# Performance work log

Measured on AMD Instinct MI355X. Metric: run time of the kernel, lower is better.

Reference implementation:

```python
import jax, jax.numpy as jnp
import numpy as np

NUM_HEADS = 8
T = 8  # hardcoded temporal dim in the original forward
MD = 3  # max_displacement -> 7x7 window
EPS = 1e-12  # F.normalize eps


def l2_normalize(x, axis):
    n = jnp.sqrt(jnp.sum(x * x, axis=axis, keepdims=True))
    return x / jnp.maximum(n, EPS)


def correlation_7x7(q, k):
    # q, k: [B, C, H, W]; FlowNet-style correlation, kernel_size=1, max_disp=3.
    # out[b, u, v, h, w] = sum_c q[b,c,h,w] * k[b,c,h+u-3,w+v-3] (zero padded)
    B, C, H, W = q.shape
    kp = jnp.pad(k, ((0, 0), (0, 0), (MD, MD), (MD, MD)))
    outs = []
    for dy in range(2 * MD + 1):
        for dx in range(2 * MD + 1):
            ks = kp[:, :, dy:dy + H, dx:dx + W]
            outs.append(jnp.sum(q * ks, axis=1))  # [B, H, W]
    corr = jnp.stack(outs, axis=1)  # [B, 49, H, W]
    return corr.reshape(B, 2 * MD + 1, 2 * MD + 1, H, W)


def setup_inputs() -> dict:
    key = jax.random.key(0)
    ks = jax.random.split(key, 6)
    B, N, C = 8, 8192, 256
    hd = C // NUM_HEADS
    std = 0.02
    return {
        "x": jax.random.normal(ks[0], (B, N, C), dtype=jnp.float32),
        "w_qk": jax.random.normal(ks[1], (2 * C, C), dtype=jnp.float32) * std,
        "w_corr": jax.random.normal(ks[2], (hd, 49), dtype=jnp.float32) * std,
        "b_corr": jnp.zeros((hd,), dtype=jnp.float32),
        "w_proj": jax.random.normal(ks[3], (C, C), dtype=jnp.float32) * std,
        "b_proj": jnp.zeros((C,), dtype=jnp.float32),
    }


def reference(x, w_qk, w_corr, b_corr, w_proj, b_proj):
    B, N, C = x.shape
    nh = NUM_HEADS
    hd = C // nh
    H = int(np.sqrt(N // T))
    W = H

    # qk projection (no bias): [B, N, 2C] -> q, k each [B, nh, N, hd]
    qk = jnp.einsum('bnc,dc->bnd', x, w_qk)
    qk = qk.reshape(B, N, 2, nh, hd).transpose(2, 0, 3, 1, 4)
    q, k = qk[0], qk[1]

    # 'b n (t h w) d -> (b n) t d h w'
    q = q.reshape(B * nh, T, H, W, hd).transpose(0, 1, 4, 2, 3)
    k = k.reshape(B * nh, T, H, W, hd).transpose(0, 1, 4, 2, 3)

    # temporal postfix: k[t+1], last frame repeated
    k_post = jnp.concatenate([k[:, 1:], k[:, -1:]], axis=1)

    qp = q.reshape(B * nh * T, hd, H, W)
    kp = k_post.reshape(B * nh * T, hd, H, W)
    qp = l2_normalize(qp, axis=1)
    kp = l2_normalize(kp, axis=1)

    corr = correlation_7x7(qp, kp)  # [(B nh T), 7, 7, H, W]
    # 'b u v h w -> b (h w) (u v)'
    corr = corr.transpose(0, 3, 4, 1, 2).reshape(B * nh * T, H * W, 49)

    v = jnp.einsum('bpk,dk->bpd', corr, w_corr) + b_corr  # [(B nh T), HW, hd]

    # '(b n t) (h w) d -> b n (t h w) d' then 'b h n d -> b n (h d)'
    out = v.reshape(B, nh, T * H * W, hd).transpose(0, 2, 1, 3).reshape(B, N, C)
    out = jnp.einsum('bnc,dc->bnd', out, w_proj) + b_proj
    return out
```

## Files before the change

kernel.cpp:

```cpp
#include <hip/hip_runtime.h>

typedef _Float16 half8 __attribute__((ext_vector_type(8)));
typedef _Float16 half2v __attribute__((ext_vector_type(2)));
typedef float float4v __attribute__((ext_vector_type(4)));

__device__ __forceinline__ float dot2acc(unsigned a, unsigned b, float c) {
#if __has_builtin(__builtin_amdgcn_fdot2)
  return __builtin_amdgcn_fdot2(__builtin_bit_cast(half2v, a), __builtin_bit_cast(half2v, b), c, false);
#else
  half2v ha = __builtin_bit_cast(half2v, a);
  half2v hb = __builtin_bit_cast(half2v, b);
  c += (float)ha[0] * (float)hb[0];
  c += (float)ha[1] * (float)hb[1];
  return c;
#endif
}
__device__ __forceinline__ unsigned hscale(unsigned a, float s) {
  half2v ha = __builtin_bit_cast(half2v, a);
  half2v r;
  r[0] = (_Float16)((float)ha[0] * s);
  r[1] = (_Float16)((float)ha[1] * s);
  return __builtin_bit_cast(unsigned, r);
}
__device__ __forceinline__ unsigned pack2(float a, float b) {
  half2v h;
  h[0] = (_Float16)a;
  h[1] = (_Float16)b;
  return __builtin_bit_cast(unsigned, h);
}
__device__ __forceinline__ void gload_lds16(const void* g, void* l) {
  __builtin_amdgcn_global_load_lds((const __attribute__((address_space(1))) unsigned*)g,
                                   (__attribute__((address_space(3))) unsigned*)l, 16, 0, 0);
}

__global__ void cvt_all(const float4* __restrict__ x, const float4* __restrict__ wqk,
                        const float4* __restrict__ wpj,
                        ushort4* __restrict__ x16, ushort4* __restrict__ wqk16,
                        ushort4* __restrict__ wpj16) {
  int b = blockIdx.x;
  const float4* s;
  ushort4* d;
  int i;
  if (b < 16384) { s = x; d = x16; i = b * 256 + threadIdx.x; }
  else if (b < 16512) { s = wqk; d = wqk16; i = (b - 16384) * 256 + threadIdx.x; }
  else { s = wpj; d = wpj16; i = (b - 16512) * 256 + threadIdx.x; }
  float4 v = s[i];
  _Float16 a = (_Float16)v.x, bb = (_Float16)v.y, c = (_Float16)v.z, e = (_Float16)v.w;
  ushort4 o;
  o.x = __builtin_bit_cast(unsigned short, a);
  o.y = __builtin_bit_cast(unsigned short, bb);
  o.z = __builtin_bit_cast(unsigned short, c);
  o.w = __builtin_bit_cast(unsigned short, e);
  d[i] = o;
}

__global__ __launch_bounds__(512, 4)
void gemm_qk(const _Float16* __restrict__ A, const _Float16* __restrict__ Bw,
             _Float16* __restrict__ qo, _Float16* __restrict__ ko) {
  __shared__ _Float16 Ash[2][4096];
  __shared__ _Float16 Bsh[2][8192];
  const int tid = threadIdx.x;
  const int lane = tid & 63, w = tid >> 6;
  const int wm = w >> 2, wn = w & 3;
  const int ml = lane & 15, qd = lane >> 4;
  const int m0 = blockIdx.y * 128, n0 = blockIdx.x * 256;

  float4v acc[4][4];
  float4v z = {0.f, 0.f, 0.f, 0.f};
#pragma unroll
  for (int i = 0; i < 4; ++i)
#pragma unroll
    for (int j = 0; j < 4; ++j) acc[i][j] = z;

  const _Float16* Ap = A + (size_t)m0 * 256;
  const _Float16* Bp = Bw + (size_t)n0 * 256;
  const int rA = tid >> 2, jA = (tid & 3) ^ ((rA >> 1) & 3);
  const int rB1 = (tid + 512) >> 2, jB1 = (tid & 3) ^ ((rB1 >> 1) & 3);

  gload_lds16(Ap + rA * 256 + jA * 8, &Ash[0][(size_t)(w * 64) * 8]);
  gload_lds16(Bp + rA * 256 + jA * 8, &Bsh[0][(size_t)(w * 64) * 8]);
  gload_lds16(Bp + rB1 * 256 + jB1 * 8, &Bsh[0][(size_t)(512 + w * 64) * 8]);
  __syncthreads();

#pragma unroll
  for (int kt = 0; kt < 8; ++kt) {
    const int cur = kt & 1;
    if (kt < 7) {
      const int k0 = (kt + 1) * 32;
      const int nb = cur ^ 1;
      gload_lds16(Ap + rA * 256 + k0 + jA * 8, &Ash[nb][(size_t)(w * 64) * 8]);
      gload_lds16(Bp + rA * 256 + k0 + jA * 8, &Bsh[nb][(size_t)(w * 64) * 8]);
      gload_lds16(Bp + rB1 * 256 + k0 + jB1 * 8, &Bsh[nb][(size_t)(512 + w * 64) * 8]);
    }
    half8 af[4], bf[4];
#pragma unroll
    for (int im = 0; im < 4; ++im) {
      int rr = wm * 64 + im * 16 + ml;
      af[im] = *(const half8*)(&Ash[cur][rr * 32 + (qd ^ ((rr >> 1) & 3)) * 8]);
      int rc = wn * 64 + im * 16 + ml;
      bf[im] = *(const half8*)(&Bsh[cur][rc * 32 + (qd ^ ((rc >> 1) & 3)) * 8]);
    }
#pragma unroll
    for (int im = 0; im < 4; ++im)
#pragma unroll
      for (int in = 0; in < 4; ++in)
        acc[im][in] = __builtin_amdgcn_mfma_f32_16x16x32_f16(bf[in], af[im], acc[im][in], 0, 0, 0);
    __syncthreads();
  }

#pragma unroll
  for (int im = 0; im < 4; ++im) {
    int rowr = m0 + wm * 64 + im * 16 + ml;
    int b = rowr >> 13, n = rowr & 8191;
    int t = n >> 10, yx = n & 1023;
#pragma unroll
    for (int in = 0; in < 4; ++in) {
      int col = n0 + wn * 64 + in * 16 + qd * 4;
      int s = col >> 8, h = (col >> 5) & 7, j = col & 31;
      _Float16* dst = s ? ko : qo;
      int p = b * 64 + h * 8 + t;
      uint2 pk;
      pk.x = pack2(acc[im][in][0], acc[im][in][1]);
      pk.y = pack2(acc[im][in][2], acc[im][in][3]);
      *(uint2*)(dst + ((size_t)p * 1024 + yx) * 32 + j) = pk;
    }
  }
}

__global__ __launch_bounds__(256, 4)
void corr_kernel(const _Float16* __restrict__ q16, const _Float16* __restrict__ k16,
                 const float* __restrict__ wcorr, const float* __restrict__ bcorr,
                 _Float16* __restrict__ outp) {
  __shared__ uint4 smem[2304];
  __shared__ uint4 wcs[256];

  const int tid = threadIdx.x;
  const int bx = blockIdx.x;
  const int p = bx >> 2, tile = bx & 3;
  const int y0 = (tile >> 1) * 16, x0 = (tile & 1) * 16;
  const int b = p >> 6, h = (p >> 3) & 7, t = p & 7;
  const int pk = (t < 7) ? p + 1 : p;
  const int ty = tid >> 4, tx = tid & 15;

  _Float16* wch = (_Float16*)wcs;
  for (int idx = tid; idx < 2048; idx += 256) {
    int d = idx >> 6, kk = idx & 63;
    float v = (kk < 49) ? wcorr[d * 49 + kk] : (kk == 49 ? bcorr[d] : 0.f);
    wch[idx] = (_Float16)v;
  }

  const _Float16* kbase = k16 + (size_t)pk * 32768;
#pragma unroll
  for (int i = 0; i < 8; ++i) {
    int g = tid + i * 256;
    if (g < 1936) {
      int vec = g >> 2, part = g & 3;
      int ky = vec / 22, kx = vec - ky * 22;
      int gy = y0 + ky - 3, gx = x0 + kx - 3;
      uint4 val = make_uint4(0u, 0u, 0u, 0u);
      if (gy >= 0 && gy < 32 && gx >= 0 && gx < 32)
        val = *(const uint4*)(kbase + ((size_t)gy * 32 + gx) * 32 + part * 8);
      int slot = (vec << 2) | (part ^ (vec & 3) ^ ((vec >> 2) & 3));
      smem[slot] = val;
    }
  }
  __syncthreads();

  for (int v = tid; v < 484; v += 256) {
    int base = v << 2;
    int sw = (v & 3) ^ ((v >> 2) & 3);
    uint4 gg[4];
#pragma unroll
    for (int pq = 0; pq < 4; ++pq) gg[pq] = smem[base | (pq ^ sw)];
    float ss = 0.f;
#pragma unroll
    for (int pq = 0; pq < 4; ++pq) {
      const unsigned* u = (const unsigned*)&gg[pq];
#pragma unroll
      for (int e = 0; e < 4; ++e) ss = dot2acc(u[e], u[e], ss);
    }
    float sc = 1.f / fmaxf(sqrtf(ss), 1e-12f);
#pragma unroll
    for (int pq = 0; pq < 4; ++pq) {
      unsigned* u = (unsigned*)&gg[pq];
#pragma unroll
      for (int e = 0; e < 4; ++e) u[e] = hscale(u[e], sc);
      smem[base | (pq ^ sw)] = gg[pq];
    }
  }
  __syncthreads();

  const _Float16* qptr = q16 + (size_t)p * 32768 + ((size_t)(y0 + ty) * 32 + (x0 + tx)) * 32;
  uint4 qv[4];
#pragma unroll
  for (int i = 0; i < 4; ++i) qv[i] = *(const uint4*)(qptr + i * 8);
  unsigned* qu = (unsigned*)qv;
  float qss = 0.f;
#pragma unroll
  for (int e = 0; e < 16; ++e) qss = dot2acc(qu[e], qu[e], qss);
  float qsc = 1.f / fmaxf(sqrtf(qss), 1e-12f);
#pragma unroll
  for (int e = 0; e < 16; ++e) qu[e] = hscale(qu[e], qsc);

  float corr[49];
#pragma unroll
  for (int dy = 0; dy < 7; ++dy) {
#pragma unroll
    for (int dx = 0; dx < 7; ++dx) {
      int vec = (ty + dy) * 22 + (tx + dx);
      int base = vec << 2;
      int sw = (vec & 3) ^ ((vec >> 2) & 3);
      float c = 0.f;
#pragma unroll
      for (int pq = 0; pq < 4; ++pq) {
        uint4 kk = smem[base | (pq ^ sw)];
        const unsigned* ku = (const unsigned*)&kk;
#pragma unroll
        for (int e = 0; e < 4; ++e) c = dot2acc(qu[pq * 4 + e], ku[e], c);
      }
      corr[dy * 7 + dx] = c;
    }
  }
  __syncthreads();

#pragma unroll
  for (int i = 0; i < 8; ++i) {
    uint4 val;
    unsigned* vu = (unsigned*)&val;
#pragma unroll
    for (int e = 0; e < 4; ++e) {
      int idx = i * 8 + e * 2;
      half2v hh;
      hh[0] = (_Float16)(idx < 49 ? corr[idx] : (idx == 49 ? 1.f : 0.f));
      hh[1] = (_Float16)(idx + 1 < 49 ? corr[idx + 1] : (idx + 1 == 49 ? 1.f : 0.f));
      vu[e] = __builtin_bit_cast(unsigned, hh);
    }
    smem[tid * 9 + i] = val;
  }
  __syncthreads();

  _Float16* corrm = (_Float16*)smem;
  const int lane = tid & 63, w = tid >> 6;
  const int ml = lane & 15, qd = lane >> 4;
  float4v vacc[4][2];
  float4v z = {0.f, 0.f, 0.f, 0.f};
#pragma unroll
  for (int im = 0; im < 4; ++im) { vacc[im][0] = z; vacc[im][1] = z; }
#pragma unroll
  for (int ks = 0; ks < 2; ++ks) {
    half8 bfrag[2];
#pragma unroll
    for (int nt = 0; nt < 2; ++nt)
      bfrag[nt] = *(const half8*)(wch + (nt * 16 + ml) * 64 + ks * 32 + qd * 8);
#pragma unroll
    for (int im = 0; im < 4; ++im) {
      half8 afrag = *(const half8*)(corrm + (w * 64 + im * 16 + ml) * 72 + ks * 32 + qd * 8);
#pragma unroll
      for (int nt = 0; nt < 2; ++nt)
        vacc[im][nt] = __builtin_amdgcn_mfma_f32_16x16x32_f16(afrag, bfrag[nt], vacc[im][nt], 0, 0, 0);
    }
  }

#pragma unroll
  for (int im = 0; im < 4; ++im) {
#pragma unroll
    for (int nt = 0; nt < 2; ++nt) {
      int d = nt * 16 + ml;
#pragma unroll
      for (int r = 0; r < 4; ++r) {
        int pos = w * 64 + im * 16 + qd * 4 + r;
        int py = pos >> 4, px = pos & 15;
        int n = t * 1024 + (y0 + py) * 32 + (x0 + px);
        outp[(((size_t)b * 8192 + n) << 8) + h * 32 + d] = (_Float16)vacc[im][nt][r];
      }
    }
  }
}

__global__ __launch_bounds__(512, 4)
void gemm_proj(const _Float16* __restrict__ A, const _Float16* __restrict__ Bw,
               const float* __restrict__ bp, float* __restrict__ out) {
  __shared__ _Float16 Ash[2][4096];
  __shared__ _Float16 Bsh[2][8192];
  const int tid = threadIdx.x;
  const int lane = tid & 63, w = tid >> 6;
  const int wm = w >> 2, wn = w & 3;
  const int ml = lane & 15, qd = lane >> 4;
  const int m0 = blockIdx.x * 128;

  float4v acc[4][4];
  float4v z = {0.f, 0.f, 0.f, 0.f};
#pragma unroll
  for (int i = 0; i < 4; ++i)
#pragma unroll
    for (int j = 0; j < 4; ++j) acc[i][j] = z;

  const _Float16* Ap = A + (size_t)m0 * 256;
  const _Float16* Bp = Bw;
  const int rA = tid >> 2, jA = (tid & 3) ^ ((rA >> 1) & 3);
  const int rB1 = (tid + 512) >> 2, jB1 = (tid & 3) ^ ((rB1 >> 1) & 3);

  gload_lds16(Ap + rA * 256 + jA * 8, &Ash[0][(size_t)(w * 64) * 8]);
  gload_lds16(Bp + rA * 256 + jA * 8, &Bsh[0][(size_t)(w * 64) * 8]);
  gload_lds16(Bp + rB1 * 256 + jB1 * 8, &Bsh[0][(size_t)(512 + w * 64) * 8]);
  __syncthreads();

#pragma unroll
  for (int kt = 0; kt < 8; ++kt) {
    const int cur = kt & 1;
    if (kt < 7) {
      const int k0 = (kt + 1) * 32;
      const int nb = cur ^ 1;
      gload_lds16(Ap + rA * 256 + k0 + jA * 8, &Ash[nb][(size_t)(w * 64) * 8]);
      gload_lds16(Bp + rA * 256 + k0 + jA * 8, &Bsh[nb][(size_t)(w * 64) * 8]);
      gload_lds16(Bp + rB1 * 256 + k0 + jB1 * 8, &Bsh[nb][(size_t)(512 + w * 64) * 8]);
    }
    half8 af[4], bf[4];
#pragma unroll
    for (int im = 0; im < 4; ++im) {
      int rr = wm * 64 + im * 16 + ml;
      af[im] = *(const half8*)(&Ash[cur][rr * 32 + (qd ^ ((rr >> 1) & 3)) * 8]);
      int rc = wn * 64 + im * 16 + ml;
      bf[im] = *(const half8*)(&Bsh[cur][rc * 32 + (qd ^ ((rc >> 1) & 3)) * 8]);
    }
#pragma unroll
    for (int im = 0; im < 4; ++im)
#pragma unroll
      for (int in = 0; in < 4; ++in)
        acc[im][in] = __builtin_amdgcn_mfma_f32_16x16x32_f16(bf[in], af[im], acc[im][in], 0, 0, 0);
    __syncthreads();
  }

#pragma unroll
  for (int im = 0; im < 4; ++im) {
    int rowr = m0 + wm * 64 + im * 16 + ml;
#pragma unroll
    for (int in = 0; in < 4; ++in) {
      int col = wn * 64 + in * 16 + qd * 4;
      float4 bb = *(const float4*)(bp + col);
      float4 o;
      o.x = acc[im][in][0] + bb.x;
      o.y = acc[im][in][1] + bb.y;
      o.z = acc[im][in][2] + bb.z;
      o.w = acc[im][in][3] + bb.w;
      *(float4*)(out + (size_t)rowr * 256 + col) = o;
    }
  }
}

extern "C" void kernel_launch(void* const* d_in, const int* in_sizes, int n_in,
                              void* d_out, int out_size, void* d_ws, size_t ws_size,
                              hipStream_t stream) {
  const float* x      = (const float*)d_in[0];
  const float* w_qk   = (const float*)d_in[1];
  const float* w_corr = (const float*)d_in[2];
  const float* b_corr = (const float*)d_in[3];
  const float* w_proj = (const float*)d_in[4];
  const float* b_proj = (const float*)d_in[5];
  float* out = (float*)d_out;

  char* ws = (char*)d_ws;
  _Float16* x16   = (_Float16*)(ws);
  _Float16* q16   = (_Float16*)(ws + 33554432);
  _Float16* k16   = (_Float16*)(ws + 67108864);
  _Float16* op16  = (_Float16*)(ws + 100663296);
  _Float16* wqk16 = (_Float16*)(ws + 134217728);
  _Float16* wpj16 = (_Float16*)(ws + 134479872);

  cvt_all<<<16576, 256, 0, stream>>>((const float4*)x, (const float4*)w_qk, (const float4*)w_proj,
                                     (ushort4*)x16, (ushort4*)wqk16, (ushort4*)wpj16);
  gemm_qk<<<dim3(2, 512), 512, 0, stream>>>(x16, wqk16, q16, k16);
  corr_kernel<<<2048, 256, 0, stream>>>(q16, k16, w_corr, b_corr, op16);
  gemm_proj<<<512, 512, 0, stream>>>(op16, wpj16, b_proj, out);
}
```

Measured before the change: 225.5 us.

## Fuse x fp32-to-fp16 conversion and L2 normalization into QK GEMM

The fp32 input x is now loaded directly inside the QK GEMM, converted to fp16 in registers and written into the LDS A tile. This removes the separate conversion pass over x and its fp16 round trip through memory. The per-head L2 normalization of q and k also moves into the GEMM epilogue using cross-lane shuffles, so the correlation kernel no longer renormalizes the key halo and query vectors. The cost is that the A-operand loads now go through registers instead of direct global-to-LDS loads, which adds VGPR pressure and LDS store work inside the main loop.

Measured after the change: 215.4 us. 1.05x faster.

```diff
diff --git a/kernel.cpp b/kernel.cpp
--- a/kernel.cpp
+++ b/kernel.cpp
@@ -15,13 +15,6 @@
   return c;
 #endif
 }
-__device__ __forceinline__ unsigned hscale(unsigned a, float s) {
-  half2v ha = __builtin_bit_cast(half2v, a);
-  half2v r;
-  r[0] = (_Float16)((float)ha[0] * s);
-  r[1] = (_Float16)((float)ha[1] * s);
-  return __builtin_bit_cast(unsigned, r);
-}
 __device__ __forceinline__ unsigned pack2(float a, float b) {
   half2v h;
   h[0] = (_Float16)a;
@@ -33,17 +26,14 @@
                                    (__attribute__((address_space(3))) unsigned*)l, 16, 0, 0);
 }
 
-__global__ void cvt_all(const float4* __restrict__ x, const float4* __restrict__ wqk,
-                        const float4* __restrict__ wpj,
-                        ushort4* __restrict__ x16, ushort4* __restrict__ wqk16,
-                        ushort4* __restrict__ wpj16) {
+__global__ void cvt_w(const float4* __restrict__ wqk, const float4* __restrict__ wpj,
+                      ushort4* __restrict__ wqk16, ushort4* __restrict__ wpj16) {
   int b = blockIdx.x;
   const float4* s;
   ushort4* d;
   int i;
-  if (b < 16384) { s = x; d = x16; i = b * 256 + threadIdx.x; }
-  else if (b < 16512) { s = wqk; d = wqk16; i = (b - 16384) * 256 + threadIdx.x; }
-  else { s = wpj; d = wpj16; i = (b - 16512) * 256 + threadIdx.x; }
+  if (b < 128) { s = wqk; d = wqk16; i = b * 256 + threadIdx.x; }
+  else { s = wpj; d = wpj16; i = (b - 128) * 256 + threadIdx.x; }
   float4 v = s[i];
   _Float16 a = (_Float16)v.x, bb = (_Float16)v.y, c = (_Float16)v.z, e = (_Float16)v.w;
   ushort4 o;
@@ -55,7 +45,7 @@
 }
 
 __global__ __launch_bounds__(512, 4)
-void gemm_qk(const _Float16* __restrict__ A, const _Float16* __restrict__ Bw,
+void gemm_qk(const float* __restrict__ X, const _Float16* __restrict__ Bw,
              _Float16* __restrict__ qo, _Float16* __restrict__ ko) {
   __shared__ _Float16 Ash[2][4096];
   __shared__ _Float16 Bsh[2][8192];
@@ -72,25 +62,35 @@
 #pragma unroll
     for (int j = 0; j < 4; ++j) acc[i][j] = z;
 
-  const _Float16* Ap = A + (size_t)m0 * 256;
+  const float* Xp = X + (size_t)m0 * 256;
   const _Float16* Bp = Bw + (size_t)n0 * 256;
-  const int rA = tid >> 2, jA = (tid & 3) ^ ((rA >> 1) & 3);
+  const int ar = tid >> 2, aj = tid & 3;
+  const int ajx = aj ^ ((ar >> 1) & 3);
+  const int rB0 = tid >> 2, jB0 = (tid & 3) ^ ((rB0 >> 1) & 3);
   const int rB1 = (tid + 512) >> 2, jB1 = (tid & 3) ^ ((rB1 >> 1) & 3);
 
-  gload_lds16(Ap + rA * 256 + jA * 8, &Ash[0][(size_t)(w * 64) * 8]);
-  gload_lds16(Bp + rA * 256 + jA * 8, &Bsh[0][(size_t)(w * 64) * 8]);
+  float4 a0 = *(const float4*)(Xp + (size_t)ar * 256 + ajx * 8);
+  float4 a1 = *(const float4*)(Xp + (size_t)ar * 256 + ajx * 8 + 4);
+  gload_lds16(Bp + rB0 * 256 + jB0 * 8, &Bsh[0][(size_t)(w * 64) * 8]);
   gload_lds16(Bp + rB1 * 256 + jB1 * 8, &Bsh[0][(size_t)(512 + w * 64) * 8]);
+  {
+    half8 h;
+    h[0] = (_Float16)a0.x; h[1] = (_Float16)a0.y; h[2] = (_Float16)a0.z; h[3] = (_Float16)a0.w;
+    h[4] = (_Float16)a1.x; h[5] = (_Float16)a1.y; h[6] = (_Float16)a1.z; h[7] = (_Float16)a1.w;
+    *(half8*)(&Ash[0][ar * 32 + aj * 8]) = h;
+  }
   __syncthreads();
 
 #pragma unroll
   for (int kt = 0; kt < 8; ++kt) {
     const int cur = kt & 1;
+    float4 n0f, n1f;
     if (kt < 7) {
       const int k0 = (kt + 1) * 32;
-      const int nb = cur ^ 1;
-      gload_lds16(Ap + rA * 256 + k0 + jA * 8, &Ash[nb][(size_t)(w * 64) * 8]);
-      gload_lds16(Bp + rA * 256 + k0 + jA * 8, &Bsh[nb][(size_t)(w * 64) * 8]);
-      gload_lds16(Bp + rB1 * 256 + k0 + jB1 * 8, &Bsh[nb][(size_t)(512 + w * 64) * 8]);
+      n0f = *(const float4*)(Xp + (size_t)ar * 256 + k0 + ajx * 8);
+      n1f = *(const float4*)(Xp + (size_t)ar * 256 + k0 + ajx * 8 + 4);
+      gload_lds16(Bp + rB0 * 256 + k0 + jB0 * 8, &Bsh[cur ^ 1][(size_t)(w * 64) * 8]);
+      gload_lds16(Bp + rB1 * 256 + k0 + jB1 * 8, &Bsh[cur ^ 1][(size_t)(512 + w * 64) * 8]);
     }
     half8 af[4], bf[4];
 #pragma unroll
@@ -105,6 +105,12 @@
 #pragma unroll
       for (int in = 0; in < 4; ++in)
         acc[im][in] = __builtin_amdgcn_mfma_f32_16x16x32_f16(bf[in], af[im], acc[im][in], 0, 0, 0);
+    if (kt < 7) {
+      half8 h;
+      h[0] = (_Float16)n0f.x; h[1] = (_Float16)n0f.y; h[2] = (_Float16)n0f.z; h[3] = (_Float16)n0f.w;
+      h[4] = (_Float16)n1f.x; h[5] = (_Float16)n1f.y; h[6] = (_Float16)n1f.z; h[7] = (_Float16)n1f.w;
+      *(half8*)(&Ash[cur ^ 1][ar * 32 + aj * 8]) = h;
+    }
     __syncthreads();
   }
 
@@ -114,15 +120,29 @@
     int b = rowr >> 13, n = rowr & 8191;
     int t = n >> 10, yx = n & 1023;
 #pragma unroll
-    for (int in = 0; in < 4; ++in) {
-      int col = n0 + wn * 64 + in * 16 + qd * 4;
-      int s = col >> 8, h = (col >> 5) & 7, j = col & 31;
-      _Float16* dst = s ? ko : qo;
-      int p = b * 64 + h * 8 + t;
-      uint2 pk;
-      pk.x = pack2(acc[im][in][0], acc[im][in][1]);
-      pk.y = pack2(acc[im][in][2], acc[im][in][3]);
-      *(uint2*)(dst + ((size_t)p * 1024 + yx) * 32 + j) = pk;
+    for (int hh = 0; hh < 2; ++hh) {
+      float ss = 0.f;
+#pragma unroll
+      for (int ii = 0; ii < 2; ++ii) {
+        int in = hh * 2 + ii;
+#pragma unroll
+        for (int r = 0; r < 4; ++r) ss += acc[im][in][r] * acc[im][in][r];
+      }
+      ss += __shfl_xor(ss, 16);
+      ss += __shfl_xor(ss, 32);
+      float sc = 1.f / fmaxf(sqrtf(ss), 1e-12f);
+#pragma unroll
+      for (int ii = 0; ii < 2; ++ii) {
+        int in = hh * 2 + ii;
+        int col = n0 + wn * 64 + in * 16 + qd * 4;
+        int s = col >> 8, h = (col >> 5) & 7, j = col & 31;
+        _Float16* dst = s ? ko : qo;
+        int p = b * 64 + h * 8 + t;
+        uint2 pk;
+        pk.x = pack2(acc[im][in][0] * sc, acc[im][in][1] * sc);
+        pk.y = pack2(acc[im][in][2] * sc, acc[im][in][3] * sc);
+        *(uint2*)(dst + ((size_t)p * 1024 + yx) * 32 + j) = pk;
+      }
     }
   }
 }
@@ -164,43 +184,13 @@
       smem[slot] = val;
     }
   }
-  __syncthreads();
-
-  for (int v = tid; v < 484; v += 256) {
-    int base = v << 2;
-    int sw = (v & 3) ^ ((v >> 2) & 3);
-    uint4 gg[4];
-#pragma unroll
-    for (int pq = 0; pq < 4; ++pq) gg[pq] = smem[base | (pq ^ sw)];
-    float ss = 0.f;
-#pragma unroll
-    for (int pq = 0; pq < 4; ++pq) {
-      const unsigned* u = (const unsigned*)&gg[pq];
-#pragma unroll
-      for (int e = 0; e < 4; ++e) ss = dot2acc(u[e], u[e], ss);
-    }
-    float sc = 1.f / fmaxf(sqrtf(ss), 1e-12f);
-#pragma unroll
-    for (int pq = 0; pq < 4; ++pq) {
-      unsigned* u = (unsigned*)&gg[pq];
-#pragma unroll
-      for (int e = 0; e < 4; ++e) u[e] = hscale(u[e], sc);
-      smem[base | (pq ^ sw)] = gg[pq];
-    }
-  }
-  __syncthreads();
 
   const _Float16* qptr = q16 + (size_t)p * 32768 + ((size_t)(y0 + ty) * 32 + (x0 + tx)) * 32;
   uint4 qv[4];
 #pragma unroll
   for (int i = 0; i < 4; ++i) qv[i] = *(const uint4*)(qptr + i * 8);
   unsigned* qu = (unsigned*)qv;
-  float qss = 0.f;
-#pragma unroll
-  for (int e = 0; e < 16; ++e) qss = dot2acc(qu[e], qu[e], qss);
-  float qsc = 1.f / fmaxf(sqrtf(qss), 1e-12f);
-#pragma unroll
-  for (int e = 0; e < 16; ++e) qu[e] = hscale(qu[e], qsc);
+  __syncthreads();
 
   float corr[49];
 #pragma unroll
@@ -360,16 +350,15 @@
   float* out = (float*)d_out;
 
   char* ws = (char*)d_ws;
-  _Float16* x16   = (_Float16*)(ws);
   _Float16* q16   = (_Float16*)(ws + 33554432);
   _Float16* k16   = (_Float16*)(ws + 67108864);
   _Float16* op16  = (_Float16*)(ws + 100663296);
   _Float16* wqk16 = (_Float16*)(ws + 134217728);
   _Float16* wpj16 = (_Float16*)(ws + 134479872);
 
-  cvt_all<<<16576, 256, 0, stream>>>((const float4*)x, (const float4*)w_qk, (const float4*)w_proj,
-                                     (ushort4*)x16, (ushort4*)wqk16, (ushort4*)wpj16);
-  gemm_qk<<<dim3(2, 512), 512, 0, stream>>>(x16, wqk16, q16, k16);
+  cvt_w<<<192, 256, 0, stream>>>((const float4*)w_qk, (const float4*)w_proj,
+                                 (ushort4*)wqk16, (ushort4*)wpj16);
+  gemm_qk<<<dim3(2, 512), 512, 0, stream>>>(x, wqk16, q16, k16);
   corr_kernel<<<2048, 256, 0, stream>>>(q16, k16, w_corr, b_corr, op16);
   gemm_proj<<<512, 512, 0, stream>>>(op16, wpj16, b_proj, out);
 }
```
